# Performance work log

Measured on AMD Instinct MI355X. Metric: run time of the kernel, lower is better.

## Reference

```python
import jax, jax.numpy as jnp
import numpy as np

N = 50000      # nodes
E = 800000     # edges (avg degree 16)
IN = 128       # in_channels
H = 8          # heads (layer 1)
C = 32         # hidden_channels per head
OUT = 40       # out_channels + 1
NEG_SLOPE = 0.2  # PyG GATConv default


def glorot(key, shape, fan_in, fan_out):
    lim = np.sqrt(6.0 / (fan_in + fan_out)).astype(np.float32)
    return jax.random.uniform(key, shape, jnp.float32, -lim, lim)


def setup_inputs() -> dict:
    key = jax.random.key(0)
    ks = jax.random.split(key, 10)
    x = jax.random.normal(ks[0], (N, IN), jnp.float32)
    edge_index = jax.random.randint(ks[1], (2, E), 0, N, dtype=jnp.int32)
    # layer 1: in -> H*C, heads=8, concat
    W1 = glorot(ks[2], (IN, H * C), IN, H * C)
    att_src1 = glorot(ks[3], (H, C), C, C)
    att_dst1 = glorot(ks[4], (H, C), C, C)
    b1 = jnp.zeros((H * C,), jnp.float32)
    # layer 2: H*C -> OUT, heads=1
    W2 = glorot(ks[5], (H * C, OUT), H * C, OUT)
    att_src2 = glorot(ks[6], (1, OUT), OUT, OUT)
    att_dst2 = glorot(ks[7], (1, OUT), OUT, OUT)
    b2 = jnp.zeros((OUT,), jnp.float32)
    return {"x": x, "edge_index": edge_index, "W1": W1, "att_src1": att_src1,
            "att_dst1": att_dst1, "b1": b1, "W2": W2, "att_src2": att_src2,
            "att_dst2": att_dst2, "b2": b2}


def gat_conv(x, edge_index, W, att_src, att_dst, bias):
    # PyG GATConv (eval mode, add_self_loops=True, concat=True)
    n = x.shape[0]
    heads, ch = att_src.shape
    loop = jnp.arange(n, dtype=edge_index.dtype)
    src = jnp.concatenate([edge_index[0], loop])  # message source j
    dst = jnp.concatenate([edge_index[1], loop])  # message target i
    h = (x @ W).reshape(n, heads, ch)                       # [N,H,C]
    a_src = jnp.einsum('nhc,hc->nh', h, att_src)            # [N,H]
    a_dst = jnp.einsum('nhc,hc->nh', h, att_dst)            # [N,H]
    logits = jax.nn.leaky_relu(a_src[src] + a_dst[dst], NEG_SLOPE)  # [Et,H]
    # segmented softmax over incoming edges of each target node
    m = jax.ops.segment_max(logits, dst, num_segments=n)    # [N,H]
    p = jnp.exp(logits - m[dst])
    s = jax.ops.segment_sum(p, dst, num_segments=n)         # [N,H]
    alpha = p / s[dst]                                      # [Et,H]
    msg = h[src] * alpha[:, :, None]                        # [Et,H,C]
    out = jax.ops.segment_sum(msg, dst, num_segments=n)     # [N,H,C]
    return out.reshape(n, heads * ch) + bias


def reference(x, edge_index, W1, att_src1, att_dst1, b1, W2, att_src2, att_dst2, b2):
    h = gat_conv(x, edge_index, W1, att_src1, att_dst1, b1)
    h = jax.nn.relu(h)  # dropout is identity in eval mode
    h = gat_conv(h, edge_index, W2, att_src2, att_dst2, b2)
    return jax.nn.log_softmax(h, axis=1)
```

## Files before the change

### kernel.cpp

```cpp
#include <hip/hip_runtime.h>
#include <hip/hip_bf16.h>
#include <math.h>

#define NEG_SLOPE 0.2f

__device__ __forceinline__ float lrelu(float x){ return x > 0.f ? x : NEG_SLOPE * x; }
__device__ __forceinline__ unsigned short f2bf(float f){
  __hip_bfloat16 h = __float2bfloat16(f);
  return __builtin_bit_cast(unsigned short, h);
}
__device__ __forceinline__ float b2f(unsigned short u){
  return __builtin_bit_cast(float, (unsigned)u << 16);
}

typedef short bf16x8 __attribute__((ext_vector_type(8)));
typedef float f32x4 __attribute__((ext_vector_type(4)));

__global__ void k_count(const int* __restrict__ dst, int* __restrict__ deg, int E){
  int e = blockIdx.x*256 + threadIdx.x;
  if (e < E) atomicAdd(&deg[dst[e]], 1);
}

__global__ __launch_bounds__(256) void k_scan1(const int* __restrict__ deg, int* __restrict__ bsum, int n){
  int tid = threadIdx.x;
  int base = blockIdx.x*1024 + tid*4;
  int s = 0;
  #pragma unroll
  for (int j=0;j<4;j++){ int idx = base+j; if (idx < n) s += deg[idx]; }
  #pragma unroll
  for (int off=32; off; off>>=1) s += __shfl_xor(s, off);
  __shared__ int ws[4];
  if ((tid&63)==0) ws[tid>>6] = s;
  __syncthreads();
  if (tid==0) bsum[blockIdx.x] = ws[0]+ws[1]+ws[2]+ws[3];
}

__global__ void k_scan2(const int* __restrict__ bsum, int* __restrict__ boff,
                        int* __restrict__ rowptr, int nb, int n){
  int lane = threadIdx.x;
  int v = (lane < nb) ? bsum[lane] : 0;
  int inc = v;
  #pragma unroll
  for (int off=1; off<64; off<<=1){ int t = __shfl_up(inc, off); if (lane >= off) inc += t; }
  if (lane < nb) boff[lane] = inc - v;
  if (lane == 63) rowptr[n] = inc;
}

__global__ __launch_bounds__(256) void k_scan3(const int* __restrict__ deg, const int* __restrict__ boff,
    int* __restrict__ rowptr, int* __restrict__ nxt, int n){
  int tid = threadIdx.x; int lane = tid & 63, w = tid >> 6;
  int base = blockIdx.x*1024 + tid*4;
  int v[4]; int s = 0;
  #pragma unroll
  for (int j=0;j<4;j++){ int idx = base+j; v[j] = (idx < n) ? deg[idx] : 0; s += v[j]; }
  int inc = s;
  #pragma unroll
  for (int off=1; off<64; off<<=1){ int t = __shfl_up(inc, off); if (lane >= off) inc += t; }
  __shared__ int ws[4];
  if (lane == 63) ws[w] = inc;
  __syncthreads();
  int run = boff[blockIdx.x];
  for (int ww=0; ww<w; ww++) run += ws[ww];
  run += inc - s;
  #pragma unroll
  for (int j=0;j<4;j++){ int idx = base+j; if (idx < n){ rowptr[idx] = run; nxt[idx] = run; run += v[j]; } }
}

__global__ void k_scatter(const int* __restrict__ src, const int* __restrict__ dst,
                          int* __restrict__ nxt, int* __restrict__ srcs, int E){
  int e = blockIdx.x*256 + threadIdx.x;
  if (e < E){
    int pos = atomicAdd(&nxt[dst[e]], 1);
    srcs[pos] = src[e];
  }
}

__global__ void k_f2b(const float* __restrict__ a, unsigned short* __restrict__ b, int n4){
  int id = blockIdx.x*256 + threadIdx.x;
  if (id < n4){
    float4 v = ((const float4*)a)[id];
    ushort4 o; o.x = f2bf(v.x); o.y = f2bf(v.y); o.z = f2bf(v.z); o.w = f2bf(v.w);
    ((ushort4*)b)[id] = o;
  }
}

__global__ void k_wt(const float* __restrict__ W, unsigned short* __restrict__ Wt, int NCreal){
  int c = blockIdx.x, k = threadIdx.x, K = blockDim.x;
  float v = (c < NCreal) ? W[(size_t)k*NCreal + c] : 0.f;
  Wt[(size_t)c*K + k] = f2bf(v);
}

__global__ __launch_bounds__(256) void gemm_mfma(
    const unsigned short* __restrict__ A, const unsigned short* __restrict__ Bt,
    unsigned short* __restrict__ C, int M, int K, int ldc){
  __shared__ unsigned short sA[64][40];
  __shared__ unsigned short sB[64][40];
  const int tid = threadIdx.x;
  const int wid = tid >> 6, lane = tid & 63;
  const int r0 = blockIdx.x * 64, c0 = blockIdx.y * 64;
  const int wr = wid >> 1, wc = wid & 1;
  const int lr = tid >> 2;
  const int lk = (tid & 3) * 8;
  const int fr = lane & 15, fk = (lane >> 4) * 8;
  f32x4 acc[2][2] = {};

  for (int k0 = 0; k0 < K; k0 += 32){
    uint4 va = make_uint4(0,0,0,0);
    int row = r0 + lr;
    if (row < M) va = *(const uint4*)(A + (size_t)row*K + k0 + lk);
    *(uint4*)&sA[lr][lk] = va;
    uint4 vb = *(const uint4*)(Bt + (size_t)(c0 + lr)*K + k0 + lk);
    *(uint4*)&sB[lr][lk] = vb;
    __syncthreads();
    bf16x8 a0 = *(const bf16x8*)&sA[wr*32 + fr][fk];
    bf16x8 a1 = *(const bf16x8*)&sA[wr*32 + 16 + fr][fk];
    bf16x8 b0 = *(const bf16x8*)&sB[wc*32 + fr][fk];
    bf16x8 b1 = *(const bf16x8*)&sB[wc*32 + 16 + fr][fk];
    acc[0][0] = __builtin_amdgcn_mfma_f32_16x16x32_bf16(a0, b0, acc[0][0], 0,0,0);
    acc[0][1] = __builtin_amdgcn_mfma_f32_16x16x32_bf16(a0, b1, acc[0][1], 0,0,0);
    acc[1][0] = __builtin_amdgcn_mfma_f32_16x16x32_bf16(a1, b0, acc[1][0], 0,0,0);
    acc[1][1] = __builtin_amdgcn_mfma_f32_16x16x32_bf16(a1, b1, acc[1][1], 0,0,0);
    __syncthreads();
  }
  #pragma unroll
  for (int mi=0; mi<2; mi++){
    int rowb = r0 + wr*32 + mi*16 + (lane>>4)*4;
    #pragma unroll
    for (int ni=0; ni<2; ni++){
      int col = c0 + wc*32 + ni*16 + fr;
      #pragma unroll
      for (int j=0;j<4;j++){
        int row = rowb + j;
        if (row < M) C[(size_t)row*ldc + col] = f2bf(acc[mi][ni][j]);
      }
    }
  }
}

__global__ void k_att1(const unsigned short* __restrict__ h, const float* __restrict__ att_s,
    const float* __restrict__ att_d, float* __restrict__ asrc, float* __restrict__ adst, int n){
  int id = blockIdx.x*256 + threadIdx.x;
  if (id >= n*8) return;
  int hd = id & 7;
  const unsigned short* hv = h + (size_t)(id>>3)*256 + hd*32;
  const float* sa = att_s + hd*32;
  const float* da = att_d + hd*32;
  float s = 0.f, d = 0.f;
  #pragma unroll
  for (int q=0; q<4; q++){
    ushort4 u0 = ((const ushort4*)hv)[q*2];
    ushort4 u1 = ((const ushort4*)hv)[q*2+1];
    float v0=b2f(u0.x), v1=b2f(u0.y), v2=b2f(u0.z), v3=b2f(u0.w);
    float v4=b2f(u1.x), v5=b2f(u1.y), v6=b2f(u1.z), v7=b2f(u1.w);
    float4 a0 = ((const float4*)sa)[q*2], a1 = ((const float4*)sa)[q*2+1];
    float4 d0 = ((const float4*)da)[q*2], d1 = ((const float4*)da)[q*2+1];
    s += v0*a0.x + v1*a0.y + v2*a0.z + v3*a0.w + v4*a1.x + v5*a1.y + v6*a1.z + v7*a1.w;
    d += v0*d0.x + v1*d0.y + v2*d0.z + v3*d0.w + v4*d1.x + v5*d1.y + v6*d1.z + v7*d1.w;
  }
  asrc[id] = s; adst[id] = d;
}

__global__ void k_att2(const unsigned short* __restrict__ h, const float* __restrict__ att_s,
    const float* __restrict__ att_d, float* __restrict__ asrc, float* __restrict__ adst, int n){
  int id = blockIdx.x*256 + threadIdx.x;
  if (id >= n) return;
  const unsigned short* hv = h + (size_t)id*64;
  float s = 0.f, d = 0.f;
  #pragma unroll
  for (int q=0; q<5; q++){
    ushort4 u0 = ((const ushort4*)hv)[q*2];
    ushort4 u1 = ((const ushort4*)hv)[q*2+1];
    float v0=b2f(u0.x), v1=b2f(u0.y), v2=b2f(u0.z), v3=b2f(u0.w);
    float v4=b2f(u1.x), v5=b2f(u1.y), v6=b2f(u1.z), v7=b2f(u1.w);
    float4 a0 = ((const float4*)att_s)[q*2], a1 = ((const float4*)att_s)[q*2+1];
    float4 d0 = ((const float4*)att_d)[q*2], d1 = ((const float4*)att_d)[q*2+1];
    s += v0*a0.x + v1*a0.y + v2*a0.z + v3*a0.w + v4*a1.x + v5*a1.y + v6*a1.z + v7*a1.w;
    d += v0*d0.x + v1*d0.y + v2*d0.z + v3*d0.w + v4*d1.x + v5*d1.y + v6*d1.z + v7*d1.w;
  }
  asrc[id] = s; adst[id] = d;
}

__global__ __launch_bounds__(256) void k_agg1(
    const unsigned short* __restrict__ h1, const float* __restrict__ asrc,
    const float* __restrict__ adst, const int* __restrict__ rowptr,
    const int* __restrict__ srcs, const float* __restrict__ bias,
    unsigned short* __restrict__ zb, int n){
  int wid = (blockIdx.x*256 + threadIdx.x) >> 6;
  int lane = threadIdx.x & 63;
  if (wid >= n) return;
  int i = wid;
  int hd = lane >> 3;
  float adsti = adst[(size_t)i*8 + hd];
  float m = lrelu(asrc[(size_t)i*8 + hd] + adsti);
  float ssum = 1.f;
  uint2 hs = ((const uint2*)(h1 + (size_t)i*256))[lane];
  float4 acc;
  acc.x = b2f((unsigned short)(hs.x & 0xffff));
  acc.y = b2f((unsigned short)(hs.x >> 16));
  acc.z = b2f((unsigned short)(hs.y & 0xffff));
  acc.w = b2f((unsigned short)(hs.y >> 16));
  int e0 = rowptr[i], e1 = rowptr[i+1];
  int e = e0;
  for (; e + 8 <= e1; e += 8){
    int sx[8]; uint2 vv[8]; float ll[8];
    #pragma unroll
    for (int j=0;j<8;j++) sx[j] = srcs[e+j];
    #pragma unroll
    for (int j=0;j<8;j++) vv[j] = ((const uint2*)(h1 + (size_t)sx[j]*256))[lane];
    #pragma unroll
    for (int j=0;j<8;j++) ll[j] = lrelu(asrc[(size_t)sx[j]*8 + hd] + adsti);
    float gm = ll[0];
    #pragma unroll
    for (int j=1;j<8;j++) gm = fmaxf(gm, ll[j]);
    float mn = fmaxf(m, gm);
    float r = __expf(m - mn); m = mn;
    ssum *= r; acc.x *= r; acc.y *= r; acc.z *= r; acc.w *= r;
    #pragma unroll
    for (int j=0;j<8;j++){
      float p = __expf(ll[j] - m);
      ssum += p;
      acc.x += p * b2f((unsigned short)(vv[j].x & 0xffff));
      acc.y += p * b2f((unsigned short)(vv[j].x >> 16));
      acc.z += p * b2f((unsigned short)(vv[j].y & 0xffff));
      acc.w += p * b2f((unsigned short)(vv[j].y >> 16));
    }
  }
  for (; e < e1; ++e){
    int s = srcs[e];
    uint2 v = ((const uint2*)(h1 + (size_t)s*256))[lane];
    float l = lrelu(asrc[(size_t)s*8 + hd] + adsti);
    float mn = fmaxf(m, l);
    float r = __expf(m - mn);
    float p = __expf(l - mn); m = mn;
    ssum = ssum*r + p;
    acc.x = acc.x*r + p * b2f((unsigned short)(v.x & 0xffff));
    acc.y = acc.y*r + p * b2f((unsigned short)(v.x >> 16));
    acc.z = acc.z*r + p * b2f((unsigned short)(v.y & 0xffff));
    acc.w = acc.w*r + p * b2f((unsigned short)(v.y >> 16));
  }
  float inv = 1.f / ssum;
  float4 b = ((const float4*)bias)[lane];
  ushort4 ob;
  ob.x = f2bf(fmaxf(fmaf(acc.x, inv, b.x), 0.f));
  ob.y = f2bf(fmaxf(fmaf(acc.y, inv, b.y), 0.f));
  ob.z = f2bf(fmaxf(fmaf(acc.z, inv, b.z), 0.f));
  ob.w = f2bf(fmaxf(fmaf(acc.w, inv, b.w), 0.f));
  ((ushort4*)(zb + (size_t)i*256))[lane] = ob;
}

__global__ __launch_bounds__(256) void k_agg2(
    const unsigned short* __restrict__ h2, const float* __restrict__ asrc,
    const float* __restrict__ adst, const int* __restrict__ rowptr,
    const int* __restrict__ srcs, const float* __restrict__ bias,
    float* __restrict__ out, int n){
  int wid = (blockIdx.x*256 + threadIdx.x) >> 6;
  int lane = threadIdx.x & 63;
  if (wid >= n) return;
  int i = wid;
  bool act = lane < 40;
  float adsti = adst[i];
  float m = lrelu(asrc[i] + adsti);
  float ssum = 1.f;
  float acc = b2f(h2[(size_t)i*64 + lane]);
  int e0 = rowptr[i], e1 = rowptr[i+1];
  int e = e0;
  for (; e + 8 <= e1; e += 8){
    int sx[8]; float vv[8], ll[8];
    #pragma unroll
    for (int j=0;j<8;j++) sx[j] = srcs[e+j];
    #pragma unroll
    for (int j=0;j<8;j++) vv[j] = b2f(h2[(size_t)sx[j]*64 + lane]);
    #pragma unroll
    for (int j=0;j<8;j++) ll[j] = lrelu(asrc[sx[j]] + adsti);
    float gm = ll[0];
    #pragma unroll
    for (int j=1;j<8;j++) gm = fmaxf(gm, ll[j]);
    float mn = fmaxf(m, gm);
    float r = __expf(m - mn); m = mn;
    ssum *= r; acc *= r;
    #pragma unroll
    for (int j=0;j<8;j++){
      float p = __expf(ll[j] - m);
      ssum += p;
      acc += p * vv[j];
    }
  }
  for (; e < e1; ++e){
    int s = srcs[e];
    float v = b2f(h2[(size_t)s*64 + lane]);
    float l = lrelu(asrc[s] + adsti);
    float mn = fmaxf(m, l);
    float r = __expf(m - mn);
    float p = __expf(l - mn); m = mn;
    ssum = ssum*r + p;
    acc  = acc*r + p*v;
  }
  float val = act ? (acc/ssum + bias[lane]) : -INFINITY;
  float mx = val;
  #pragma unroll
  for (int off=32; off; off>>=1) mx = fmaxf(mx, __shfl_xor(mx, off));
  float ex = act ? __expf(val - mx) : 0.f;
  float se = ex;
  #pragma unroll
  for (int off=32; off; off>>=1) se += __shfl_xor(se, off);
  if (act) out[(size_t)i*40 + lane] = val - mx - __logf(se);
}

extern "C" void kernel_launch(void* const* d_in, const int* in_sizes, int n_in,
                              void* d_out, int out_size, void* d_ws, size_t ws_size,
                              hipStream_t stream){
  const float* x   = (const float*)d_in[0];
  const int*   ei  = (const int*)d_in[1];
  const float* W1  = (const float*)d_in[2];
  const float* as1 = (const float*)d_in[3];
  const float* ad1 = (const float*)d_in[4];
  const float* b1  = (const float*)d_in[5];
  const float* W2  = (const float*)d_in[6];
  const float* as2 = (const float*)d_in[7];
  const float* ad2 = (const float*)d_in[8];
  const float* b2  = (const float*)d_in[9];
  float* out = (float*)d_out;

  const int N = in_sizes[0] / 128;
  const int E = in_sizes[1] / 2;
  const int* srcI = ei;
  const int* dstI = ei + E;

  char* ws = (char*)d_ws;
  size_t off = 0;
  auto alloc = [&](size_t bytes){ void* p = ws + off; off += (bytes + 255) & ~(size_t)255; return p; };
  unsigned short* h1b = (unsigned short*)alloc((size_t)N*256*2);
  unsigned short* xb  = (unsigned short*)alloc((size_t)N*128*2);
  unsigned short* zb  = (unsigned short*)alloc((size_t)N*256*2);
  unsigned short* h2b = (unsigned short*)alloc((size_t)N*64*2);
  unsigned short* W1t = (unsigned short*)alloc((size_t)256*128*2);
  unsigned short* W2t = (unsigned short*)alloc((size_t)64*256*2);
  float* asrc1 = (float*)alloc((size_t)N*8*4);
  float* adst1 = (float*)alloc((size_t)N*8*4);
  float* asrc2 = (float*)alloc((size_t)N*4);
  float* adst2 = (float*)alloc((size_t)N*4);
  int* deg     = (int*)alloc((size_t)N*4);
  int* rowptr  = (int*)alloc((size_t)(N+1)*4);
  int* nxt     = (int*)alloc((size_t)N*4);
  int* srcs    = (int*)alloc((size_t)E*4);
  int* bsum    = (int*)alloc(256*4);
  int* boff    = (int*)alloc(256*4);
  (void)ws_size; (void)n_in; (void)out_size;

  const int nb = (N + 1023)/1024;
  hipMemsetAsync(deg, 0, (size_t)N*4, stream);
  int eb = (E + 255)/256;
  k_count <<<eb, 256, 0, stream>>>(dstI, deg, E);
  k_scan1 <<<nb, 256, 0, stream>>>(deg, bsum, N);
  k_scan2 <<<1, 64, 0, stream>>>(bsum, boff, rowptr, nb, N);
  k_scan3 <<<nb, 256, 0, stream>>>(deg, boff, rowptr, nxt, N);
  k_scatter<<<eb, 256, 0, stream>>>(srcI, dstI, nxt, srcs, E);

  k_f2b<<<((N*128/4) + 255)/256, 256, 0, stream>>>(x, xb, N*128/4);
  k_wt <<<256, 128, 0, stream>>>(W1, W1t, 256);
  k_wt <<<64, 256, 0, stream>>>(W2, W2t, 40);

  dim3 g1((N + 63)/64, 4);
  gemm_mfma<<<g1, 256, 0, stream>>>(xb, W1t, h1b, N, 128, 256);
  k_att1<<<(N*8 + 255)/256, 256, 0, stream>>>(h1b, as1, ad1, asrc1, adst1, N);
  k_agg1<<<(N + 3)/4, 256, 0, stream>>>(h1b, asrc1, adst1, rowptr, srcs, b1, zb, N);

  dim3 g2((N + 63)/64, 1);
  gemm_mfma<<<g2, 256, 0, stream>>>(zb, W2t, h2b, N, 256, 64);
  k_att2<<<(N + 255)/256, 256, 0, stream>>>(h2b, as2, ad2, asrc2, adst2, N);
  k_agg2<<<(N + 3)/4, 256, 0, stream>>>(h2b, asrc2, adst2, rowptr, srcs, b2, out, N);
}
```

Measured before the change: 340.2 us.

## Fuse fp32-to-bf16 conversion and attention logits into layer-1 GEMM; split agg1 per half

Layer 1 now runs as a single GEMM kernel that reads fp32 x directly and converts it to bf16 while staging into shared memory, so the separate conversion kernel and its bf16 copy of x disappear. Each block covers all 256 output columns and computes the per-head att_src/att_dst dot products from the accumulators with a cross-lane shuffle reduction, which removes k_att1 and its re-read of h1. Aggregation for layer 1 now uses two wavefronts per node, each handling 4 heads, to expose more parallelism for the gathers. In exchange, each GEMM block holds more accumulators and shared memory, which may lower occupancy, and agg1 issues narrower gather loads.

```diff
diff --git a/kernel.cpp b/kernel.cpp
--- a/kernel.cpp
+++ b/kernel.cpp
@@ -75,19 +75,92 @@
   }
 }
 
-__global__ void k_f2b(const float* __restrict__ a, unsigned short* __restrict__ b, int n4){
-  int id = blockIdx.x*256 + threadIdx.x;
-  if (id < n4){
-    float4 v = ((const float4*)a)[id];
-    ushort4 o; o.x = f2bf(v.x); o.y = f2bf(v.y); o.z = f2bf(v.z); o.w = f2bf(v.w);
-    ((ushort4*)b)[id] = o;
-  }
-}
-
 __global__ void k_wt(const float* __restrict__ W, unsigned short* __restrict__ Wt, int NCreal){
   int c = blockIdx.x, k = threadIdx.x, K = blockDim.x;
   float v = (c < NCreal) ? W[(size_t)k*NCreal + c] : 0.f;
   Wt[(size_t)c*K + k] = f2bf(v);
+}
+
+__global__ __launch_bounds__(256) void gemm1_att(
+    const float* __restrict__ x, const unsigned short* __restrict__ Bt,
+    unsigned short* __restrict__ C, const float* __restrict__ att_s,
+    const float* __restrict__ att_d, float* __restrict__ asrc,
+    float* __restrict__ adst, int M){
+  __shared__ unsigned short sA[64][40];
+  __shared__ unsigned short sB[256][40];
+  const int tid = threadIdx.x;
+  const int wid = tid >> 6, lane = tid & 63;
+  const int r0 = blockIdx.x * 64;
+  const int fr = lane & 15, fk = (lane >> 4) * 8;
+  f32x4 acc[4][4] = {};
+
+  for (int k0 = 0; k0 < 128; k0 += 32){
+    #pragma unroll
+    for (int t=0; t<2; t++){
+      int id = tid + t*256;
+      int r = id >> 3, q = id & 7;
+      float4 v = make_float4(0.f,0.f,0.f,0.f);
+      int row = r0 + r;
+      if (row < M) v = ((const float4*)(x + (size_t)row*128))[(k0>>2) + q];
+      ushort4 o; o.x=f2bf(v.x); o.y=f2bf(v.y); o.z=f2bf(v.z); o.w=f2bf(v.w);
+      *(ushort4*)&sA[r][q*4] = o;
+    }
+    #pragma unroll
+    for (int t=0; t<4; t++){
+      int id = tid + t*256;
+      int r = id >> 2, lk = (id & 3) * 8;
+      uint4 vb = *(const uint4*)(Bt + (size_t)r*128 + k0 + lk);
+      *(uint4*)&sB[r][lk] = vb;
+    }
+    __syncthreads();
+    bf16x8 a[4], b[4];
+    #pragma unroll
+    for (int mi=0; mi<4; mi++) a[mi] = *(const bf16x8*)&sA[mi*16 + fr][fk];
+    #pragma unroll
+    for (int ni=0; ni<4; ni++) b[ni] = *(const bf16x8*)&sB[wid*64 + ni*16 + fr][fk];
+    #pragma unroll
+    for (int mi=0; mi<4; mi++)
+      #pragma unroll
+      for (int ni=0; ni<4; ni++)
+        acc[mi][ni] = __builtin_amdgcn_mfma_f32_16x16x32_bf16(a[mi], b[ni], acc[mi][ni], 0,0,0);
+    __syncthreads();
+  }
+
+  float avs[4], avd[4];
+  #pragma unroll
+  for (int ni=0; ni<4; ni++){
+    int idx = (2*wid + (ni>>1))*32 + (ni&1)*16 + fr;
+    avs[ni] = att_s[idx];
+    avd[ni] = att_d[idx];
+  }
+
+  #pragma unroll
+  for (int mi=0; mi<4; mi++){
+    #pragma unroll
+    for (int j=0; j<4; j++){
+      int row = r0 + mi*16 + (lane>>4)*4 + j;
+      #pragma unroll
+      for (int ni=0; ni<4; ni++){
+        int col = wid*64 + ni*16 + fr;
+        if (row < M) C[(size_t)row*256 + col] = f2bf(acc[mi][ni][j]);
+      }
+      float s0 = acc[mi][0][j]*avs[0] + acc[mi][1][j]*avs[1];
+      float s1 = acc[mi][2][j]*avs[2] + acc[mi][3][j]*avs[3];
+      float d0 = acc[mi][0][j]*avd[0] + acc[mi][1][j]*avd[1];
+      float d1 = acc[mi][2][j]*avd[2] + acc[mi][3][j]*avd[3];
+      #pragma unroll
+      for (int mk=1; mk<16; mk<<=1){
+        s0 += __shfl_xor(s0, mk); s1 += __shfl_xor(s1, mk);
+        d0 += __shfl_xor(d0, mk); d1 += __shfl_xor(d1, mk);
+      }
+      if ((lane & 15) == 0 && row < M){
+        asrc[(size_t)row*8 + 2*wid    ] = s0;
+        asrc[(size_t)row*8 + 2*wid + 1] = s1;
+        adst[(size_t)row*8 + 2*wid    ] = d0;
+        adst[(size_t)row*8 + 2*wid + 1] = d1;
+      }
+    }
+  }
 }
 
 __global__ __launch_bounds__(256) void gemm_mfma(
@@ -137,29 +210,6 @@
   }
 }
 
-__global__ void k_att1(const unsigned short* __restrict__ h, const float* __restrict__ att_s,
-    const float* __restrict__ att_d, float* __restrict__ asrc, float* __restrict__ adst, int n){
-  int id = blockIdx.x*256 + threadIdx.x;
-  if (id >= n*8) return;
-  int hd = id & 7;
-  const unsigned short* hv = h + (size_t)(id>>3)*256 + hd*32;
-  const float* sa = att_s + hd*32;
-  const float* da = att_d + hd*32;
-  float s = 0.f, d = 0.f;
-  #pragma unroll
-  for (int q=0; q<4; q++){
-    ushort4 u0 = ((const ushort4*)hv)[q*2];
-    ushort4 u1 = ((const ushort4*)hv)[q*2+1];
-    float v0=b2f(u0.x), v1=b2f(u0.y), v2=b2f(u0.z), v3=b2f(u0.w);
-    float v4=b2f(u1.x), v5=b2f(u1.y), v6=b2f(u1.z), v7=b2f(u1.w);
-    float4 a0 = ((const float4*)sa)[q*2], a1 = ((const float4*)sa)[q*2+1];
-    float4 d0 = ((const float4*)da)[q*2], d1 = ((const float4*)da)[q*2+1];
-    s += v0*a0.x + v1*a0.y + v2*a0.z + v3*a0.w + v4*a1.x + v5*a1.y + v6*a1.z + v7*a1.w;
-    d += v0*d0.x + v1*d0.y + v2*d0.z + v3*d0.w + v4*d1.x + v5*d1.y + v6*d1.z + v7*d1.w;
-  }
-  asrc[id] = s; adst[id] = d;
-}
-
 __global__ void k_att2(const unsigned short* __restrict__ h, const float* __restrict__ att_s,
     const float* __restrict__ att_d, float* __restrict__ asrc, float* __restrict__ adst, int n){
   int id = blockIdx.x*256 + threadIdx.x;
@@ -185,28 +235,25 @@
     const float* __restrict__ adst, const int* __restrict__ rowptr,
     const int* __restrict__ srcs, const float* __restrict__ bias,
     unsigned short* __restrict__ zb, int n){
-  int wid = (blockIdx.x*256 + threadIdx.x) >> 6;
+  int gw = (blockIdx.x*256 + threadIdx.x) >> 6;
   int lane = threadIdx.x & 63;
-  if (wid >= n) return;
-  int i = wid;
-  int hd = lane >> 3;
+  int i = gw >> 1, half = gw & 1;
+  if (i >= n) return;
+  int hd = half*4 + (lane >> 4);
   float adsti = adst[(size_t)i*8 + hd];
   float m = lrelu(asrc[(size_t)i*8 + hd] + adsti);
   float ssum = 1.f;
-  uint2 hs = ((const uint2*)(h1 + (size_t)i*256))[lane];
-  float4 acc;
-  acc.x = b2f((unsigned short)(hs.x & 0xffff));
-  acc.y = b2f((unsigned short)(hs.x >> 16));
-  acc.z = b2f((unsigned short)(hs.y & 0xffff));
-  acc.w = b2f((unsigned short)(hs.y >> 16));
+  unsigned hv = ((const unsigned*)(h1 + (size_t)i*256))[half*64 + lane];
+  float accx = b2f((unsigned short)(hv & 0xffff));
+  float accy = b2f((unsigned short)(hv >> 16));
   int e0 = rowptr[i], e1 = rowptr[i+1];
   int e = e0;
   for (; e + 8 <= e1; e += 8){
-    int sx[8]; uint2 vv[8]; float ll[8];
+    int sx[8]; unsigned vv[8]; float ll[8];
     #pragma unroll
     for (int j=0;j<8;j++) sx[j] = srcs[e+j];
     #pragma unroll
-    for (int j=0;j<8;j++) vv[j] = ((const uint2*)(h1 + (size_t)sx[j]*256))[lane];
+    for (int j=0;j<8;j++) vv[j] = ((const unsigned*)(h1 + (size_t)sx[j]*256))[half*64 + lane];
     #pragma unroll
     for (int j=0;j<8;j++) ll[j] = lrelu(asrc[(size_t)sx[j]*8 + hd] + adsti);
     float gm = ll[0];
@@ -214,38 +261,31 @@
     for (int j=1;j<8;j++) gm = fmaxf(gm, ll[j]);
     float mn = fmaxf(m, gm);
     float r = __expf(m - mn); m = mn;
-    ssum *= r; acc.x *= r; acc.y *= r; acc.z *= r; acc.w *= r;
+    ssum *= r; accx *= r; accy *= r;
     #pragma unroll
     for (int j=0;j<8;j++){
       float p = __expf(ll[j] - m);
       ssum += p;
-      acc.x += p * b2f((unsigned short)(vv[j].x & 0xffff));
-      acc.y += p * b2f((unsigned short)(vv[j].x >> 16));
-      acc.z += p * b2f((unsigned short)(vv[j].y & 0xffff));
-      acc.w += p * b2f((unsigned short)(vv[j].y >> 16));
+      accx += p * b2f((unsigned short)(vv[j] & 0xffff));
+      accy += p * b2f((unsigned short)(vv[j] >> 16));
     }
   }
   for (; e < e1; ++e){
     int s = srcs[e];
-    uint2 v = ((const uint2*)(h1 + (size_t)s*256))[lane];
+    unsigned v = ((const unsigned*)(h1 + (size_t)s*256))[half*64 + lane];
     float l = lrelu(asrc[(size_t)s*8 + hd] + adsti);
     float mn = fmaxf(m, l);
     float r = __expf(m - mn);
     float p = __expf(l - mn); m = mn;
     ssum = ssum*r + p;
-    acc.x = acc.x*r + p * b2f((unsigned short)(v.x & 0xffff));
-    acc.y = acc.y*r + p * b2f((unsigned short)(v.x >> 16));
-    acc.z = acc.z*r + p * b2f((unsigned short)(v.y & 0xffff));
-    acc.w = acc.w*r + p * b2f((unsigned short)(v.y >> 16));
+    accx = accx*r + p * b2f((unsigned short)(v & 0xffff));
+    accy = accy*r + p * b2f((unsigned short)(v >> 16));
   }
   float inv = 1.f / ssum;
-  float4 b = ((const float4*)bias)[lane];
-  ushort4 ob;
-  ob.x = f2bf(fmaxf(fmaf(acc.x, inv, b.x), 0.f));
-  ob.y = f2bf(fmaxf(fmaf(acc.y, inv, b.y), 0.f));
-  ob.z = f2bf(fmaxf(fmaf(acc.z, inv, b.z), 0.f));
-  ob.w = f2bf(fmaxf(fmaf(acc.w, inv, b.w), 0.f));
-  ((ushort4*)(zb + (size_t)i*256))[lane] = ob;
+  float2 b = ((const float2*)bias)[half*64 + lane];
+  unsigned ob = (unsigned)f2bf(fmaxf(fmaf(accx, inv, b.x), 0.f))
+              | ((unsigned)f2bf(fmaxf(fmaf(accy, inv, b.y), 0.f)) << 16);
+  ((unsigned*)(zb + (size_t)i*256))[half*64 + lane] = ob;
 }
 
 __global__ __launch_bounds__(256) void k_agg2(
@@ -330,7 +370,6 @@
   size_t off = 0;
   auto alloc = [&](size_t bytes){ void* p = ws + off; off += (bytes + 255) & ~(size_t)255; return p; };
   unsigned short* h1b = (unsigned short*)alloc((size_t)N*256*2);
-  unsigned short* xb  = (unsigned short*)alloc((size_t)N*128*2);
   unsigned short* zb  = (unsigned short*)alloc((size_t)N*256*2);
   unsigned short* h2b = (unsigned short*)alloc((size_t)N*64*2);
   unsigned short* W1t = (unsigned short*)alloc((size_t)256*128*2);
@@ -356,14 +395,11 @@
   k_scan3 <<<nb, 256, 0, stream>>>(deg, boff, rowptr, nxt, N);
   k_scatter<<<eb, 256, 0, stream>>>(srcI, dstI, nxt, srcs, E);
 
-  k_f2b<<<((N*128/4) + 255)/256, 256, 0, stream>>>(x, xb, N*128/4);
   k_wt <<<256, 128, 0, stream>>>(W1, W1t, 256);
   k_wt <<<64, 256, 0, stream>>>(W2, W2t, 40);
 
-  dim3 g1((N + 63)/64, 4);
-  gemm_mfma<<<g1, 256, 0, stream>>>(xb, W1t, h1b, N, 128, 256);
-  k_att1<<<(N*8 + 255)/256, 256, 0, stream>>>(h1b, as1, ad1, asrc1, adst1, N);
-  k_agg1<<<(N + 3)/4, 256, 0, stream>>>(h1b, asrc1, adst1, rowptr, srcs, b1, zb, N);
+  gemm1_att<<<(N + 63)/64, 256, 0, stream>>>(x, W1t, h1b, as1, ad1, asrc1, adst1, N);
+  k_agg1<<<(2*N + 3)/4, 256, 0, stream>>>(h1b, asrc1, adst1, rowptr, srcs, b1, zb, N);
 
   dim3 g2((N + 63)/64, 1);
   gemm_mfma<<<g2, 256, 0, stream>>>(zb, W2t, h2b, N, 256, 64);
```

After: 350.8 us. +3.1%, slower.
